# Kernel tuning notes

Hardware: AMD Instinct MI355X
Metric: run time of the kernel (lower is better)

Reference implementation:

```python
import jax, jax.numpy as jnp
import numpy as np

B, T, M, S, D, H, DH, P = 4, 1024, 1024, 1024, 1024, 16, 64, 4096


def layernorm(x, g, b, eps=1e-5):
    mu = x.mean(-1, keepdims=True)
    var = ((x - mu) ** 2).mean(-1, keepdims=True)
    return (x - mu) * jax.lax.rsqrt(var + eps) * g + b


def rel_shift(x):
    # Transformer-XL relative shift on [B,H,q,k] BD scores
    b, h, q, k = x.shape
    x = jnp.pad(x, ((0, 0), (0, 0), (0, 0), (1, 0)))
    return x.reshape(b, h, k + 1, q)[:, :, 1:, :].reshape(b, h, q, k)


def rel_attention(x, kv, mem, mask, pos_emb, r_w_bias, r_r_bias,
                  Wq, Wk, Wv, Wr, Wo, g, bln):
    # x: [B,Tq,D] queries; kv: [B,Skv,D]; mem: optional [B,M,D]
    cat = kv if mem is None else jnp.concatenate([mem, kv], axis=1)
    Bb, Tq, _ = x.shape
    K = cat.shape[1]
    q = (x @ Wq).reshape(Bb, Tq, H, DH)
    k = (cat @ Wk).reshape(Bb, K, H, DH)
    v = (cat @ Wv).reshape(Bb, K, H, DH)
    r = (pos_emb[-K:] @ Wr).reshape(K, H, DH)  # rel-pos keys, most-recent K positions
    AC = jnp.einsum('bthd,bkhd->bhtk', q + r_w_bias, k)
    BD = rel_shift(jnp.einsum('bthd,khd->bhtk', q + r_r_bias, r))
    scores = (AC + BD) * (1.0 / np.sqrt(DH))
    scores = jnp.where(mask[:, None, :, :], jnp.asarray(-1e30, scores.dtype), scores)
    prob = jax.nn.softmax(scores, axis=-1)
    o = jnp.einsum('bhtk,bkhd->bthd', prob, v).reshape(Bb, Tq, H * DH) @ Wo
    return layernorm(x + o, g, bln), cat, prob  # post-LN residual; cat is new memory


def residual_ff(x, W1, b1, W2, b2, g, bln):
    h = jax.nn.relu(x @ W1 + b1) @ W2 + b2
    return layernorm(x + h, g, bln)


def setup_inputs() -> dict:
    key = jax.random.key(0)
    ks = jax.random.split(key, 24)
    w = lambda i, shape: jax.random.normal(ks[i], shape, jnp.float32) * 0.02
    causal = jnp.triu(jnp.ones((T, M + T), bool), k=M + 1)  # True = masked
    return {
        'src': jax.random.normal(ks[0], (B, S, D), jnp.float32),
        'tgt': jax.random.normal(ks[1], (B, T, D), jnp.float32),
        'tgt_mem': jax.random.normal(ks[2], (B, M, D), jnp.float32),
        'pos_emb': w(3, (M + T, D)),
        'r_w_bias': w(4, (H, DH)),
        'r_r_bias': w(5, (H, DH)),
        'Wq1': w(6, (D, H * DH)), 'Wk1': w(7, (D, H * DH)), 'Wv1': w(8, (D, H * DH)),
        'Wr1': w(9, (D, H * DH)), 'Wo1': w(10, (H * DH, D)),
        'ln1_g': jnp.ones((D,), jnp.float32), 'ln1_b': jnp.zeros((D,), jnp.float32),
        'Wq2': w(11, (D, H * DH)), 'Wk2': w(12, (D, H * DH)), 'Wv2': w(13, (D, H * DH)),
        'Wr2': w(14, (D, H * DH)), 'Wo2': w(15, (H * DH, D)),
        'ln2_g': jnp.ones((D,), jnp.float32), 'ln2_b': jnp.zeros((D,), jnp.float32),
        'Wf1': w(16, (D, P)), 'bf1': jnp.zeros((P,), jnp.float32),
        'Wf2': w(17, (P, D)), 'bf2': jnp.zeros((D,), jnp.float32),
        'ln3_g': jnp.ones((D,), jnp.float32), 'ln3_b': jnp.zeros((D,), jnp.float32),
        'tgt_mask': jnp.broadcast_to(causal, (B, T, M + T)),
        'tgt_to_src_mask': jnp.zeros((B, T, S), bool),
    }


def reference(src, tgt, tgt_mem, pos_emb, r_w_bias, r_r_bias,
              Wq1, Wk1, Wv1, Wr1, Wo1, ln1_g, ln1_b,
              Wq2, Wk2, Wv2, Wr2, Wo2, ln2_g, ln2_b,
              Wf1, bf1, Wf2, bf2, ln3_g, ln3_b,
              tgt_mask, tgt_to_src_mask):
    out, new_mem, self_att_prob = rel_attention(
        tgt, tgt, tgt_mem, tgt_mask, pos_emb, r_w_bias, r_r_bias,
        Wq1, Wk1, Wv1, Wr1, Wo1, ln1_g, ln1_b)
    out, _, inter_att_prob = rel_attention(
        out, src, None, tgt_to_src_mask, pos_emb, r_w_bias, r_r_bias,
        Wq2, Wk2, Wv2, Wr2, Wo2, ln2_g, ln2_b)
    out = residual_ff(out, Wf1, bf1, Wf2, bf2, ln3_g, ln3_b)
    return (out, new_mem, self_att_prob, inter_att_prob)
```

## Files before the change

kernel.cpp:

```cpp
#include <hip/hip_runtime.h>

typedef unsigned short u16;
typedef __attribute__((ext_vector_type(8))) short short8;
typedef __attribute__((ext_vector_type(4))) float f4;
typedef __attribute__((ext_vector_type(4))) unsigned short u16x4;

__device__ __forceinline__ float b2f(u16 u) {
    unsigned int x = ((unsigned int)u) << 16;
    return __builtin_bit_cast(float, x);
}
__device__ __forceinline__ u16 f2b(float f) {
    unsigned int u = __builtin_bit_cast(unsigned int, f);
    u += 0x7FFFu + ((u >> 16) & 1u);
    return (u16)(u >> 16);
}

__device__ __forceinline__ void gl16(const void* g, void* l) {
    __builtin_amdgcn_global_load_lds(
        (const __attribute__((address_space(1))) void*)g,
        (__attribute__((address_space(3))) void*)l, 16, 0, 0);
}

template<int FM, int FN, int CBF, int EPI>
__global__ __launch_bounds__(256, 3)
void gemm_bt(const u16* __restrict__ Ap, const u16* __restrict__ Bp,
             void* __restrict__ Cp, const float* __restrict__ bias,
             int M, int N, int K, int lda, int ldb, int ldc,
             long long sAh, long long sAb, long long sBh, long long sBb,
             long long sCh, long long sCb, int batchH)
{
    constexpr int BM = FM * 32;
    constexpr int BN = FN * 32;
    __shared__ __align__(16) u16 As[BM * 32];
    __shared__ __align__(16) u16 Bs[BN * 32];

    const int tid  = threadIdx.x;
    const int z    = blockIdx.z;
    const int bb   = z / batchH;
    const int hh   = z - bb * batchH;
    const int m0   = blockIdx.y * BM;
    const int n0   = blockIdx.x * BN;
    const int w    = tid >> 6;
    const int lane = tid & 63;
    const int wr   = w >> 1;
    const int wc   = w & 1;
    const int lrow = lane & 15;
    const int lk   = (lane >> 4) << 3;
    const int lrow4 = lane >> 2;
    const int lch   = lane & 3;

    const u16* Ag = Ap + sAb * bb + sAh * hh;
    const u16* Bg = Bp + sBb * bb + sBh * hh;

    f4 acc[FM][FN] = {};

    const int nKt = K >> 5;
    for (int kt = 0; kt < nKt; ++kt) {
        const int kb = kt << 5;
        __syncthreads();
        #pragma unroll
        for (int i = 0; i < BM / 64; ++i) {
            const int row0 = (w + i * 4) << 4;
            gl16(Ag + (long long)(m0 + row0 + lrow4) * lda + kb + (lch << 3),
                 &As[row0 * 32]);
        }
        #pragma unroll
        for (int i = 0; i < BN / 64; ++i) {
            const int row0 = (w + i * 4) << 4;
            gl16(Bg + (long long)(n0 + row0 + lrow4) * ldb + kb + (lch << 3),
                 &Bs[row0 * 32]);
        }
        __syncthreads();

        short8 af[FM], bv[FN];
        #pragma unroll
        for (int m = 0; m < FM; ++m)
            af[m] = *(const short8*)(&As[(wr * FM * 16 + m * 16 + lrow) * 32 + lk]);
        #pragma unroll
        for (int n = 0; n < FN; ++n)
            bv[n] = *(const short8*)(&Bs[(wc * FN * 16 + n * 16 + lrow) * 32 + lk]);
        #pragma unroll
        for (int m = 0; m < FM; ++m)
            #pragma unroll
            for (int n = 0; n < FN; ++n)
                acc[m][n] = __builtin_amdgcn_mfma_f32_16x16x32_bf16(af[m], bv[n], acc[m][n], 0, 0, 0);
    }

    const int crow0 = m0 + wr * FM * 16 + ((lane >> 4) << 2);
    const int ccol0 = n0 + wc * FN * 16 + lrow;
    if (CBF == 0) {
        float* Cg = (float*)Cp + sCb * bb + sCh * hh;
        #pragma unroll
        for (int m = 0; m < FM; ++m) {
            #pragma unroll
            for (int n = 0; n < FN; ++n) {
                const int col = ccol0 + n * 16;
                float bvv = (EPI >= 1) ? bias[col] : 0.f;
                #pragma unroll
                for (int r = 0; r < 4; ++r) {
                    float vv = acc[m][n][r] + bvv;
                    if (EPI == 2) vv = fmaxf(vv, 0.f);
                    Cg[(long long)(crow0 + m * 16 + r) * ldc + col] = vv;
                }
            }
        }
    } else {
        u16* Cg = (u16*)Cp + sCb * bb + sCh * hh;
        #pragma unroll
        for (int m = 0; m < FM; ++m) {
            #pragma unroll
            for (int n = 0; n < FN; ++n) {
                const int col = ccol0 + n * 16;
                float bvv = (EPI >= 1) ? bias[col] : 0.f;
                #pragma unroll
                for (int r = 0; r < 4; ++r) {
                    float vv = acc[m][n][r] + bvv;
                    if (EPI == 2) vv = fmaxf(vv, 0.f);
                    Cg[(long long)(crow0 + m * 16 + r) * ldc + col] = f2b(vv);
                }
            }
        }
    }
}

template<int KK, int MODE>
__global__ __launch_bounds__(512)
void fattn(const u16* __restrict__ qw, const u16* __restrict__ qr,
           const u16* __restrict__ kb, const u16* __restrict__ rr,
           const u16* __restrict__ vt,
           float* __restrict__ probs, u16* __restrict__ ob, int kld)
{
    constexpr int LE = KK + 8;
    constexpr int NT = KK / 16;
    __shared__ __align__(16) u16 e[16 * LE];
    __shared__ __align__(16) u16 qws[16 * 72];
    __shared__ __align__(16) u16 qrs[17 * 72];
    __shared__ float psum[8][16];

    const int tid = threadIdx.x;
    const int bh  = blockIdx.y;
    const int b   = bh >> 4, h = bh & 15;
    const int t0  = blockIdx.x << 4;

    if (tid < 128) {
        const int row = tid >> 3, ch = tid & 7;
        *(short8*)&qws[row * 72 + ch * 8] =
            *(const short8*)(qw + ((long long)(b * 1024 + t0 + row)) * 1024 + h * 64 + ch * 8);
    } else if (tid < 256) {
        const int row = (tid - 128) >> 3, ch = tid & 7;
        *(short8*)&qrs[row * 72 + ch * 8] =
            *(const short8*)(qr + ((long long)(b * 1024 + t0 + row)) * 1024 + h * 64 + ch * 8);
    } else if (MODE == 1 && tid < 264) {
        const int ch = tid - 256;
        const int trow = (t0 + 16 > 1023) ? 1023 : (t0 + 16);
        *(short8*)&qrs[16 * 72 + ch * 8] =
            *(const short8*)(qr + ((long long)(b * 1024 + trow)) * 1024 + h * 64 + ch * 8);
    }
    __syncthreads();

    const int w = tid >> 6, lane = tid & 63;
    const int lc = lane & 15, g = lane >> 4, lk = g << 3;
    const int t = t0 + lc;

    const short8 bq0 = *(const short8*)&qws[lc * 72 + lk];
    const short8 bq1 = *(const short8*)&qws[lc * 72 + 32 + lk];
    const short8 br0 = *(const short8*)&qrs[lc * 72 + lk];
    const short8 br1 = *(const short8*)&qrs[lc * 72 + 32 + lk];
    short8 bs0 = {}, bs1 = {};
    if (MODE == 1) {
        bs0 = *(const short8*)&qrs[(lc + 1) * 72 + lk];
        bs1 = *(const short8*)&qrs[(lc + 1) * 72 + 32 + lk];
    }

    for (int ut = w; ut < NT; ut += 8) {
        const int u0 = ut << 4;
        const bool need1 = (u0 + t0 + 30 >= 1023);
        const bool need2 = (MODE == 1) && (u0 + t0 <= 1021);
        if (!need1 && !need2) continue;
        const u16* rg = rr + (long long)(u0 + lc) * 2048 + h * 64;
        const short8 a0 = *(const short8*)(rg + lk);
        const short8 a1 = *(const short8*)(rg + 32 + lk);
        if (need1) {
            f4 acc = {};
            acc = __builtin_amdgcn_mfma_f32_16x16x32_bf16(a0, br0, acc, 0, 0, 0);
            acc = __builtin_amdgcn_mfma_f32_16x16x32_bf16(a1, br1, acc, 0, 0, 0);
            #pragma unroll
            for (int i = 0; i < 4; ++i) {
                const int j = u0 + 4 * g + i + t - 1023;
                if (j >= 0) e[lc * LE + j] = f2b(acc[i]);
            }
        }
        if (MODE == 1 && need2) {
            f4 acc = {};
            acc = __builtin_amdgcn_mfma_f32_16x16x32_bf16(a0, bs0, acc, 0, 0, 0);
            acc = __builtin_amdgcn_mfma_f32_16x16x32_bf16(a1, bs1, acc, 0, 0, 0);
            #pragma unroll
            for (int i = 0; i < 4; ++i) {
                const int j = u0 + 4 * g + i + t + 2;
                if (j < KK) e[lc * LE + j] = f2b(acc[i]);
            }
        }
    }
    __syncthreads();

    float sum = 0.f;
    const int limit = t + 1024;
    const int jvt = (MODE == 0) ? ((t0 + 1039) >> 4) : (NT - 1);
    #pragma unroll 2
    for (int jt = w; jt < NT; jt += 8) {
        const int j0 = jt << 4;
        const int jme = j0 + 4 * g;
        if (MODE == 0 && jt > jvt) {
            u16x4 z = {0, 0, 0, 0};
            *(u16x4*)&e[lc * LE + jme] = z;
            continue;
        }
        const u16* kg = kb + (long long)(b * KK + j0 + lc) * kld + h * 64;
        const short8 a0 = *(const short8*)(kg + lk);
        const short8 a1 = *(const short8*)(kg + 32 + lk);
        f4 acc = {};
        acc = __builtin_amdgcn_mfma_f32_16x16x32_bf16(a0, bq0, acc, 0, 0, 0);
        acc = __builtin_amdgcn_mfma_f32_16x16x32_bf16(a1, bq1, acc, 0, 0, 0);
        u16x4 bd4 = *(const u16x4*)&e[lc * LE + jme];
        u16x4 st;
        #pragma unroll
        for (int i = 0; i < 4; ++i) {
            const int j = jme + i;
            float bd = b2f(bd4[i]);
            if (MODE == 1 && j == t + 1) bd = 0.f;
            float ev = __expf(acc[i] + bd);
            if (MODE == 0 && j > limit) ev = 0.f;
            sum += ev;
            st[i] = f2b(ev);
        }
        *(u16x4*)&e[lc * LE + jme] = st;
    }
    sum += __shfl_xor(sum, 16);
    sum += __shfl_xor(sum, 32);
    if (g == 0) psum[w][lc] = sum;
    __syncthreads();

    if (w >= 4) {
        const int r = (tid >> 4) & 15;
        const int q = tid & 15;
        float s = 0.f;
        #pragma unroll
        for (int w2 = 0; w2 < 8; ++w2) s += psum[w2][r];
        const float inv = 1.f / s;
        float* pr = probs + ((long long)bh * 1024 + t0 + r) * KK;
        #pragma unroll 4
        for (int i2 = 0; i2 < KK / 128; ++i2) {
            const int j0 = q * 8 + i2 * 128;
            u16x4 e0 = *(const u16x4*)&e[r * LE + j0];
            u16x4 e1 = *(const u16x4*)&e[r * LE + j0 + 4];
            f4 p0, p1;
            p0.x = b2f(e0.x) * inv; p0.y = b2f(e0.y) * inv;
            p0.z = b2f(e0.z) * inv; p0.w = b2f(e0.w) * inv;
            p1.x = b2f(e1.x) * inv; p1.y = b2f(e1.y) * inv;
            p1.z = b2f(e1.z) * inv; p1.w = b2f(e1.w) * inv;
            *(f4*)(pr + j0) = p0;
            *(f4*)(pr + j0 + 4) = p1;
        }
    } else {
        const int db = w << 4;
        const u16* vrow = vt + ((long long)(bh * 64 + db + lc)) * KK + lk;
        int kcend = KK / 32;
        if (MODE == 0) {
            const int ke = (t0 + 1071) >> 5;
            if (ke < kcend) kcend = ke;
        }
        f4 acc = {};
        #pragma unroll 2
        for (int kc = 0; kc < kcend; ++kc) {
            short8 a = *(const short8*)&e[lc * LE + kc * 32 + lk];
            short8 bv = *(const short8*)(vrow + kc * 32);
            acc = __builtin_amdgcn_mfma_f32_16x16x32_bf16(a, bv, acc, 0, 0, 0);
        }
        #pragma unroll
        for (int i = 0; i < 4; ++i) {
            const int trow = g * 4 + i;
            float s = 0.f;
            #pragma unroll
            for (int w2 = 0; w2 < 8; ++w2) s += psum[w2][trow];
            ob[((long long)(b * 1024 + t0 + trow)) * 1024 + h * 64 + db + lc] = f2b(acc[i] / s);
        }
    }
}

__global__ void conv_f2b(const float* __restrict__ in, u16* __restrict__ out, long long n4)
{
    long long i = (long long)blockIdx.x * 256 + threadIdx.x;
    if (i >= n4) return;
    f4 v = *(const f4*)(in + i * 4);
    u16x4 o; o.x = f2b(v.x); o.y = f2b(v.y); o.z = f2b(v.z); o.w = f2b(v.w);
    *(u16x4*)(out + i * 4) = o;
}

__global__ void concat_mem(const float* __restrict__ mem, const float* __restrict__ tgt,
                           float* __restrict__ nm, u16* __restrict__ cat)
{
    long long i = (long long)blockIdx.x * 256 + threadIdx.x;
    long long b = i >> 19;
    int rem = (int)(i & 524287);
    int r = rem >> 8, c4 = rem & 255;
    const float* sp = (r < 1024) ? (mem + ((b << 10) + r) * 1024 + c4 * 4)
                                 : (tgt + ((b << 10) + (r - 1024)) * 1024 + c4 * 4);
    f4 v = *(const f4*)sp;
    *(f4*)(nm + i * 4) = v;
    u16x4 o; o.x = f2b(v.x); o.y = f2b(v.y); o.z = f2b(v.z); o.w = f2b(v.w);
    *(u16x4*)(cat + i * 4) = o;
}

struct TW10 { const float* s[10]; u16* d[10]; };
__global__ void transpose_w10(TW10 p)
{
    __shared__ float tile[32][33];
    const float* W = p.s[blockIdx.z];
    u16* Wt = p.d[blockIdx.z];
    int c0 = blockIdx.x * 32, r0 = blockIdx.y * 32;
    int tx = threadIdx.x, ty = threadIdx.y;
    tile[ty][tx] = W[(long long)(r0 + ty) * 1024 + c0 + tx];
    __syncthreads();
    Wt[(long long)(c0 + ty) * 1024 + r0 + tx] = f2b(tile[tx][ty]);
}

__global__ void transpose_w(const float* __restrict__ W, u16* __restrict__ Wt, int R, int C)
{
    __shared__ float tile[32][33];
    int c0 = blockIdx.x * 32, r0 = blockIdx.y * 32;
    int tx = threadIdx.x, ty = threadIdx.y;
    tile[ty][tx] = W[(long long)(r0 + ty) * C + c0 + tx];
    __syncthreads();
    Wt[(long long)(c0 + ty) * R + r0 + tx] = f2b(tile[tx][ty]);
}

__global__ void transpose_v(const u16* __restrict__ v, u16* __restrict__ vt,
                            int KK, int ld, int coff)
{
    __shared__ u16 tile[32][33];
    int z = blockIdx.z; int b = z >> 4, hh = z & 15;
    int j0 = blockIdx.x * 32, d0 = blockIdx.y * 32;
    int tx = threadIdx.x, ty = threadIdx.y;
    tile[ty][tx] = v[((long long)(b * KK + j0 + ty)) * ld + coff + hh * 64 + d0 + tx];
    __syncthreads();
    vt[((long long)((b * 16 + hh) * 64 + d0 + ty)) * KK + j0 + tx] = tile[tx][ty];
}

__global__ void add_qbias(const u16* __restrict__ src, long long ld, long long sb,
                          const float* __restrict__ rwb, const float* __restrict__ rrb,
                          u16* __restrict__ qwo, u16* __restrict__ qro)
{
    long long i = (long long)blockIdx.x * 256 + threadIdx.x;
    const int col = (int)((i * 4) & 1023);
    const long long trow = (i * 4) >> 10;
    const long long b = trow >> 10;
    const long long tr = trow & 1023;
    u16x4 qq = *(const u16x4*)(src + b * sb + tr * ld + col);
    f4 wv = *(const f4*)(rwb + col);
    f4 rv = *(const f4*)(rrb + col);
    u16x4 a, c;
    a.x = f2b((b2f(qq.x) + wv.x) * 0.125f); a.y = f2b((b2f(qq.y) + wv.y) * 0.125f);
    a.z = f2b((b2f(qq.z) + wv.z) * 0.125f); a.w = f2b((b2f(qq.w) + wv.w) * 0.125f);
    c.x = f2b((b2f(qq.x) + rv.x) * 0.125f); c.y = f2b((b2f(qq.y) + rv.y) * 0.125f);
    c.z = f2b((b2f(qq.z) + rv.z) * 0.125f); c.w = f2b((b2f(qq.w) + rv.w) * 0.125f);
    *(u16x4*)(qwo + i * 4) = a;
    *(u16x4*)(qro + i * 4) = c;
}

__global__ __launch_bounds__(256) void ln_res(const float* __restrict__ x,
                                              const float* __restrict__ h1,
                                              const float* __restrict__ h2,
                                              const float* __restrict__ hbias,
                                              const float* __restrict__ g, const float* __restrict__ bl,
                                              float* __restrict__ o32, u16* __restrict__ obf)
{
    const long long row = blockIdx.x;
    const int tid = threadIdx.x;
    const long long base = row * 1024 + tid * 4;
    f4 xa = *(const f4*)(x + base);
    f4 ha = *(const f4*)(h1 + base);
    f4 hb = *(const f4*)(h2 + base);
    f4 hc = {0.f, 0.f, 0.f, 0.f};
    if (hbias) hc = *(const f4*)(hbias + tid * 4);
    float v0 = xa.x + ha.x + hb.x + hc.x, v1 = xa.y + ha.y + hb.y + hc.y;
    float v2 = xa.z + ha.z + hb.z + hc.z, v3 = xa.w + ha.w + hb.w + hc.w;
    float lsum = v0 + v1 + v2 + v3;
    float lsq = v0 * v0 + v1 * v1 + v2 * v2 + v3 * v3;
    #pragma unroll
    for (int o2 = 32; o2; o2 >>= 1) { lsum += __shfl_xor(lsum, o2); lsq += __shfl_xor(lsq, o2); }
    __shared__ float r1[4], r2[4];
    int w = tid >> 6, lane = tid & 63;
    if (lane == 0) { r1[w] = lsum; r2[w] = lsq; }
    __syncthreads();
    lsum = r1[0] + r1[1] + r1[2] + r1[3];
    lsq  = r2[0] + r2[1] + r2[2] + r2[3];
    const float mu = lsum * 0.0009765625f;
    const float var = lsq * 0.0009765625f - mu * mu;
    const float rsd = rsqrtf(var + 1e-5f);
    const int c = tid * 4;
    f4 gv = *(const f4*)(g + c);
    f4 bv = *(const f4*)(bl + c);
    f4 y;
    y.x = (v0 - mu) * rsd * gv.x + bv.x;
    y.y = (v1 - mu) * rsd * gv.y + bv.y;
    y.z = (v2 - mu) * rsd * gv.z + bv.z;
    y.w = (v3 - mu) * rsd * gv.w + bv.w;
    *(f4*)(o32 + base) = y;
    if (obf) {
        u16x4 u; u.x = f2b(y.x); u.y = f2b(y.y); u.z = f2b(y.z); u.w = f2b(y.w);
        *(u16x4*)(obf + base) = u;
    }
}

extern "C" void kernel_launch(void* const* d_in, const int* in_sizes, int n_in,
                              void* d_out, int out_size, void* d_ws, size_t ws_size,
                              hipStream_t stream)
{
    (void)in_sizes; (void)n_in; (void)out_size;
    const float* src  = (const float*)d_in[0];
    const float* tgt  = (const float*)d_in[1];
    const float* mem  = (const float*)d_in[2];
    const float* pos  = (const float*)d_in[3];
    const float* rwb  = (const float*)d_in[4];
    const float* rrb  = (const float*)d_in[5];
    const float* Wq1  = (const float*)d_in[6];
    const float* Wk1  = (const float*)d_in[7];
    const float* Wv1  = (const float*)d_in[8];
    const float* Wr1  = (const float*)d_in[9];
    const float* Wo1  = (const float*)d_in[10];
    const float* ln1g = (const float*)d_in[11];
    const float* ln1b = (const float*)d_in[12];
    const float* Wq2  = (const float*)d_in[13];
    const float* Wk2  = (const float*)d_in[14];
    const float* Wv2  = (const float*)d_in[15];
    const float* Wr2  = (const float*)d_in[16];
    const float* Wo2  = (const float*)d_in[17];
    const float* ln2g = (const float*)d_in[18];
    const float* ln2b = (const float*)d_in[19];
    const float* Wf1  = (const float*)d_in[20];
    const float* bf1  = (const float*)d_in[21];
    const float* Wf2  = (const float*)d_in[22];
    const float* bf2  = (const float*)d_in[23];
    const float* ln3g = (const float*)d_in[24];
    const float* ln3b = (const float*)d_in[25];

    float* outp   = (float*)d_out;
    float* newmem = outp + 4194304;
    float* selfP  = outp + 12582912;
    float* interP = outp + 146800640;

    char* ws = (char*)d_ws;
    size_t off = 0;
    auto alloc = [&](size_t bytes) -> void* {
        void* p = ws + off;
        off = (off + bytes + 255) & ~(size_t)255;
        return p;
    };
    u16*   src_bf  = (u16*)alloc(8u << 20);
    u16*   cat_bf  = (u16*)alloc(16u << 20);
    u16*   pos_bf  = (u16*)alloc(4u << 20);
    u16*   W1t    = (u16*)alloc(6u << 20);
    u16*   Wr12t  = (u16*)alloc(4u << 20);
    u16*   W2t    = (u16*)alloc(4u << 20);
    u16*   Wq2t   = (u16*)alloc(2u << 20);
    u16*   Wo1t   = (u16*)alloc(2u << 20);
    u16*   Wo2t   = (u16*)alloc(2u << 20);
    u16*   Wf1t   = (u16*)alloc(8u << 20);
    u16*   Wf2t   = (u16*)alloc(8u << 20);
    u16*   P1     = (u16*)alloc(48u << 20);
    u16*   P2     = (u16*)alloc(16u << 20);
    u16*   R12    = (u16*)alloc(8u << 20);
    u16*   qwb    = (u16*)alloc(8u << 20);
    u16*   qrb    = (u16*)alloc(8u << 20);
    u16*   qb2    = (u16*)alloc(8u << 20);
    u16*   vtb    = (u16*)alloc(16u << 20);
    u16*   ob     = (u16*)alloc(8u << 20);
    float* projb  = (float*)alloc(16u << 20);
    float* projb2 = (float*)alloc(16u << 20);
    float* out1_32 = (float*)alloc(16u << 20);
    u16*   out1_bf = (u16*)alloc(8u << 20);
    float* out2_32 = (float*)alloc(16u << 20);
    u16*   out2_bf = (u16*)alloc(8u << 20);
    u16*   hb     = (u16*)alloc(32u << 20);
    if (off > ws_size) return;
    const long long PJ2 = projb2 - projb;

    dim3 tb(32, 32);

    concat_mem<<<8192, 256, 0, stream>>>(mem, tgt, newmem, cat_bf);
    conv_f2b<<<4096, 256, 0, stream>>>(src, src_bf, 1048576);
    conv_f2b<<<2048, 256, 0, stream>>>(pos, pos_bf, 524288);
    TW10 tw;
    tw.s[0] = Wq1; tw.d[0] = W1t;
    tw.s[1] = Wk1; tw.d[1] = W1t + 1048576;
    tw.s[2] = Wv1; tw.d[2] = W1t + 2097152;
    tw.s[3] = Wr1; tw.d[3] = Wr12t;
    tw.s[4] = Wr2; tw.d[4] = Wr12t + 1048576;
    tw.s[5] = Wk2; tw.d[5] = W2t;
    tw.s[6] = Wv2; tw.d[6] = W2t + 1048576;
    tw.s[7] = Wq2; tw.d[7] = Wq2t;
    tw.s[8] = Wo1; tw.d[8] = Wo1t;
    tw.s[9] = Wo2; tw.d[9] = Wo2t;
    transpose_w10<<<dim3(32, 32, 10), tb, 0, stream>>>(tw);
    transpose_w<<<dim3(128, 32), tb, 0, stream>>>(Wf1, Wf1t, 1024, 4096);
    transpose_w<<<dim3(32, 128), tb, 0, stream>>>(Wf2, Wf2t, 4096, 1024);

    gemm_bt<4,4,1,0><<<dim3(24,64,1), 256, 0, stream>>>(cat_bf, W1t, P1, nullptr,
        8192,3072,1024, 1024,1024,3072, 0,0,0,0,0,0, 1);
    gemm_bt<4,4,1,0><<<dim3(16,16,1), 256, 0, stream>>>(pos_bf, Wr12t, R12, nullptr,
        2048,2048,1024, 1024,1024,2048, 0,0,0,0,0,0, 1);
    add_qbias<<<4096, 256, 0, stream>>>(P1 + 1024LL * 3072, 3072LL, 2048LL * 3072,
                                        rwb, rrb, qwb, qrb);
    transpose_v<<<dim3(64,2,64), tb, 0, stream>>>(P1, vtb, 2048, 3072, 2048);
    fattn<2048,0><<<dim3(64,64), 512, 0, stream>>>(qwb, qrb, P1 + 1024, R12, vtb,
                                                   selfP, ob, 3072);
    gemm_bt<4,4,0,0><<<dim3(8,32,2), 256, 0, stream>>>(ob, Wo1t, projb, nullptr,
        4096,1024,512, 1024,1024,1024, 0,512, 0,512, 0,PJ2, 1);
    ln_res<<<4096, 256, 0, stream>>>(tgt, projb, projb2, nullptr, ln1g, ln1b, out1_32, out1_bf);

    gemm_bt<4,4,1,0><<<dim3(8,32,1), 256, 0, stream>>>(out1_bf, Wq2t, qb2, nullptr,
        4096,1024,1024, 1024,1024,1024, 0,0,0,0,0,0, 1);
    gemm_bt<4,4,1,0><<<dim3(16,32,1), 256, 0, stream>>>(src_bf, W2t, P2, nullptr,
        4096,2048,1024, 1024,1024,2048, 0,0,0,0,0,0, 1);
    add_qbias<<<4096, 256, 0, stream>>>(qb2, 1024LL, 1048576LL, rwb, rrb, qwb, qrb);
    transpose_v<<<dim3(32,2,64), tb, 0, stream>>>(P2, vtb, 1024, 2048, 1024);
    fattn<1024,1><<<dim3(64,64), 512, 0, stream>>>(qwb, qrb, P2,
        R12 + 1024LL * 2048 + 1024, vtb, interP, ob, 2048);
    gemm_bt<4,4,0,0><<<dim3(8,32,2), 256, 0, stream>>>(ob, Wo2t, projb, nullptr,
        4096,1024,512, 1024,1024,1024, 0,512, 0,512, 0,PJ2, 1);
    ln_res<<<4096, 256, 0, stream>>>(out1_32, projb, projb2, nullptr, ln2g, ln2b, out2_32, out2_bf);

    gemm_bt<4,4,1,2><<<dim3(32,32,1), 256, 0, stream>>>(out2_bf, Wf1t, hb, bf1,
        4096,4096,1024, 1024,1024,4096, 0,0,0,0,0,0, 1);
    gemm_bt<4,4,0,0><<<dim3(8,32,2), 256, 0, stream>>>(hb, Wf2t, projb, nullptr,
        4096,1024,2048, 4096,4096,1024, 0,2048, 0,2048, 0,PJ2, 1);
    ln_res<<<4096, 256, 0, stream>>>(out2_32, projb, projb2, bf2, ln3g, ln3b, outp, nullptr);
}
```

Baseline: 1.043 ms.

## Fuse q-bias into attention, batch weight transposes, widen V transpose tiles

The add_qbias pass is folded into the attention kernel's query staging, so the q+bias tensors are no longer written to and re-read from global memory. The separate weight-transpose launches become one 18-slice launch, and the second layer's Q, K and V projections run as one batched GEMM launch. The V transpose now uses 64x64 tiles with 16-byte vector accesses. Prob and new-memory stores become nontemporal, and unroll factors in the attention loops are raised. In exchange there is more register pressure and more work in the attention prologue.

```diff
diff --git a/kernel.cpp b/kernel.cpp
--- a/kernel.cpp
+++ b/kernel.cpp
@@ -125,7 +125,8 @@
 
 template<int KK, int MODE>
 __global__ __launch_bounds__(512)
-void fattn(const u16* __restrict__ qw, const u16* __restrict__ qr,
+void fattn(const u16* __restrict__ qsrc, long long qld, long long qsb,
+           const float* __restrict__ rwb, const float* __restrict__ rrb,
            const u16* __restrict__ kb, const u16* __restrict__ rr,
            const u16* __restrict__ vt,
            float* __restrict__ probs, u16* __restrict__ ob, int kld)
@@ -142,19 +143,28 @@
     const int b   = bh >> 4, h = bh & 15;
     const int t0  = blockIdx.x << 4;
 
-    if (tid < 128) {
-        const int row = tid >> 3, ch = tid & 7;
-        *(short8*)&qws[row * 72 + ch * 8] =
-            *(const short8*)(qw + ((long long)(b * 1024 + t0 + row)) * 1024 + h * 64 + ch * 8);
-    } else if (tid < 256) {
-        const int row = (tid - 128) >> 3, ch = tid & 7;
-        *(short8*)&qrs[row * 72 + ch * 8] =
-            *(const short8*)(qr + ((long long)(b * 1024 + t0 + row)) * 1024 + h * 64 + ch * 8);
-    } else if (MODE == 1 && tid < 264) {
-        const int ch = tid - 256;
-        const int trow = (t0 + 16 > 1023) ? 1023 : (t0 + 16);
-        *(short8*)&qrs[16 * 72 + ch * 8] =
-            *(const short8*)(qr + ((long long)(b * 1024 + trow)) * 1024 + h * 64 + ch * 8);
+    if (tid < 264) {
+        int row, ch; const float* bias; u16* dst; bool act = true;
+        if (tid < 128)      { row = tid >> 3;        ch = tid & 7; bias = rwb; dst = &qws[row * 72 + ch * 8]; }
+        else if (tid < 256) { row = (tid - 128) >> 3; ch = tid & 7; bias = rrb; dst = &qrs[row * 72 + ch * 8]; }
+        else if (MODE == 1) { row = 16;              ch = tid - 256; bias = rrb; dst = &qrs[16 * 72 + ch * 8]; }
+        else act = false;
+        if (act) {
+            int trow = t0 + row; if (trow > 1023) trow = 1023;
+            short8 qv = *(const short8*)(qsrc + b * qsb + (long long)trow * qld + h * 64 + ch * 8);
+            const float* bp = bias + h * 64 + ch * 8;
+            f4 b0 = *(const f4*)bp, b1 = *(const f4*)(bp + 4);
+            short8 o;
+            o[0] = (short)f2b((b2f((u16)qv[0]) + b0.x) * 0.125f);
+            o[1] = (short)f2b((b2f((u16)qv[1]) + b0.y) * 0.125f);
+            o[2] = (short)f2b((b2f((u16)qv[2]) + b0.z) * 0.125f);
+            o[3] = (short)f2b((b2f((u16)qv[3]) + b0.w) * 0.125f);
+            o[4] = (short)f2b((b2f((u16)qv[4]) + b1.x) * 0.125f);
+            o[5] = (short)f2b((b2f((u16)qv[5]) + b1.y) * 0.125f);
+            o[6] = (short)f2b((b2f((u16)qv[6]) + b1.z) * 0.125f);
+            o[7] = (short)f2b((b2f((u16)qv[7]) + b1.w) * 0.125f);
+            *(short8*)dst = o;
+        }
     }
     __syncthreads();
 
@@ -172,6 +182,7 @@
         bs1 = *(const short8*)&qrs[(lc + 1) * 72 + 32 + lk];
     }
 
+    #pragma unroll 2
     for (int ut = w; ut < NT; ut += 8) {
         const int u0 = ut << 4;
         const bool need1 = (u0 + t0 + 30 >= 1023);
@@ -206,7 +217,7 @@
     float sum = 0.f;
     const int limit = t + 1024;
     const int jvt = (MODE == 0) ? ((t0 + 1039) >> 4) : (NT - 1);
-    #pragma unroll 2
+    #pragma unroll 4
     for (int jt = w; jt < NT; jt += 8) {
         const int j0 = jt << 4;
         const int jme = j0 + 4 * g;
@@ -258,8 +269,8 @@
             p0.z = b2f(e0.z) * inv; p0.w = b2f(e0.w) * inv;
             p1.x = b2f(e1.x) * inv; p1.y = b2f(e1.y) * inv;
             p1.z = b2f(e1.z) * inv; p1.w = b2f(e1.w) * inv;
-            *(f4*)(pr + j0) = p0;
-            *(f4*)(pr + j0 + 4) = p1;
+            __builtin_nontemporal_store(p0, (f4*)(pr + j0));
+            __builtin_nontemporal_store(p1, (f4*)(pr + j0 + 4));
         }
     } else {
         const int db = w << 4;
@@ -306,65 +317,48 @@
     const float* sp = (r < 1024) ? (mem + ((b << 10) + r) * 1024 + c4 * 4)
                                  : (tgt + ((b << 10) + (r - 1024)) * 1024 + c4 * 4);
     f4 v = *(const f4*)sp;
-    *(f4*)(nm + i * 4) = v;
+    __builtin_nontemporal_store(v, (f4*)(nm + i * 4));
     u16x4 o; o.x = f2b(v.x); o.y = f2b(v.y); o.z = f2b(v.z); o.w = f2b(v.w);
     *(u16x4*)(cat + i * 4) = o;
 }
 
-struct TW10 { const float* s[10]; u16* d[10]; };
-__global__ void transpose_w10(TW10 p)
+struct TWS { const float* s; u16* d; int sld, dld; };
+struct TW18 { TWS t[18]; };
+__global__ void transpose_w18(TW18 p)
 {
     __shared__ float tile[32][33];
-    const float* W = p.s[blockIdx.z];
-    u16* Wt = p.d[blockIdx.z];
+    const TWS ts = p.t[blockIdx.z];
     int c0 = blockIdx.x * 32, r0 = blockIdx.y * 32;
     int tx = threadIdx.x, ty = threadIdx.y;
-    tile[ty][tx] = W[(long long)(r0 + ty) * 1024 + c0 + tx];
+    tile[ty][tx] = ts.s[(long long)(r0 + ty) * ts.sld + c0 + tx];
     __syncthreads();
-    Wt[(long long)(c0 + ty) * 1024 + r0 + tx] = f2b(tile[tx][ty]);
-}
-
-__global__ void transpose_w(const float* __restrict__ W, u16* __restrict__ Wt, int R, int C)
-{
-    __shared__ float tile[32][33];
-    int c0 = blockIdx.x * 32, r0 = blockIdx.y * 32;
-    int tx = threadIdx.x, ty = threadIdx.y;
-    tile[ty][tx] = W[(long long)(r0 + ty) * C + c0 + tx];
+    ts.d[(long long)(c0 + ty) * ts.dld + r0 + tx] = f2b(tile[tx][ty]);
+}
+
+__global__ __launch_bounds__(256) void transpose_v(const u16* __restrict__ v, u16* __restrict__ vt,
+                                                   int KK, int ld, int coff)
+{
+    __shared__ u16 tile[64][68];
+    const int z = blockIdx.z, b = z >> 4, h = z & 15;
+    const int j0 = blockIdx.x << 6;
+    const int rr8 = threadIdx.x >> 3;
+    const int c8 = (threadIdx.x & 7) << 3;
+    #pragma unroll
+    for (int p = 0; p < 2; ++p) {
+        const int jr = p * 32 + rr8;
+        short8 val = *(const short8*)(v + ((long long)(b * KK + j0 + jr)) * ld + coff + h * 64 + c8);
+        #pragma unroll
+        for (int k = 0; k < 8; ++k) tile[c8 + k][jr] = (u16)val[k];
+    }
     __syncthreads();
-    Wt[(long long)(c0 + ty) * R + r0 + tx] = f2b(tile[tx][ty]);
-}
-
-__global__ void transpose_v(const u16* __restrict__ v, u16* __restrict__ vt,
-                            int KK, int ld, int coff)
-{
-    __shared__ u16 tile[32][33];
-    int z = blockIdx.z; int b = z >> 4, hh = z & 15;
-    int j0 = blockIdx.x * 32, d0 = blockIdx.y * 32;
-    int tx = threadIdx.x, ty = threadIdx.y;
-    tile[ty][tx] = v[((long long)(b * KK + j0 + ty)) * ld + coff + hh * 64 + d0 + tx];
-    __syncthreads();
-    vt[((long long)((b * 16 + hh) * 64 + d0 + ty)) * KK + j0 + tx] = tile[tx][ty];
-}
-
-__global__ void add_qbias(const u16* __restrict__ src, long long ld, long long sb,
-                          const float* __restrict__ rwb, const float* __restrict__ rrb,
-                          u16* __restrict__ qwo, u16* __restrict__ qro)
-{
-    long long i = (long long)blockIdx.x * 256 + threadIdx.x;
-    const int col = (int)((i * 4) & 1023);
-    const long long trow = (i * 4) >> 10;
-    const long long b = trow >> 10;
-    const long long tr = trow & 1023;
-    u16x4 qq = *(const u16x4*)(src + b * sb + tr * ld + col);
-    f4 wv = *(const f4*)(rwb + col);
-    f4 rv = *(const f4*)(rrb + col);
-    u16x4 a, c;
-    a.x = f2b((b2f(qq.x) + wv.x) * 0.125f); a.y = f2b((b2f(qq.y) + wv.y) * 0.125f);
-    a.z = f2b((b2f(qq.z) + wv.z) * 0.125f); a.w = f2b((b2f(qq.w) + wv.w) * 0.125f);
-    c.x = f2b((b2f(qq.x) + rv.x) * 0.125f); c.y = f2b((b2f(qq.y) + rv.y) * 0.125f);
-    c.z = f2b((b2f(qq.z) + rv.z) * 0.125f); c.w = f2b((b2f(qq.w) + rv.w) * 0.125f);
-    *(u16x4*)(qwo + i * 4) = a;
-    *(u16x4*)(qro + i * 4) = c;
+    #pragma unroll
+    for (int p = 0; p < 2; ++p) {
+        const int d = p * 32 + rr8;
+        short8 o;
+        #pragma unroll
+        for (int k = 0; k < 8; ++k) o[k] = (short)tile[d][c8 + k];
+        *(short8*)(vt + ((long long)((b * 16 + h) * 64 + d)) * KK + j0 + c8) = o;
+    }
 }
 
 __global__ __launch_bounds__(256) void ln_res(const float* __restrict__ x,
@@ -468,10 +462,9 @@
     u16*   Wf1t   = (u16*)alloc(8u << 20);
     u16*   Wf2t   = (u16*)alloc(8u << 20);
     u16*   P1     = (u16*)alloc(48u << 20);
-    u16*   P2     = (u16*)alloc(16u << 20);
+    u16*   P2k    = (u16*)alloc(8u << 20);
+    u16*   P2v    = (u16*)alloc(8u << 20);
     u16*   R12    = (u16*)alloc(8u << 20);
-    u16*   qwb    = (u16*)alloc(8u << 20);
-    u16*   qrb    = (u16*)alloc(8u << 20);
     u16*   qb2    = (u16*)alloc(8u << 20);
     u16*   vtb    = (u16*)alloc(16u << 20);
     u16*   ob     = (u16*)alloc(8u << 20);
@@ -490,42 +483,46 @@
     concat_mem<<<8192, 256, 0, stream>>>(mem, tgt, newmem, cat_bf);
     conv_f2b<<<4096, 256, 0, stream>>>(src, src_bf, 1048576);
     conv_f2b<<<2048, 256, 0, stream>>>(pos, pos_bf, 524288);
-    TW10 tw;
-    tw.s[0] = Wq1; tw.d[0] = W1t;
-    tw.s[1] = Wk1; tw.d[1] = W1t + 1048576;
-    tw.s[2] = Wv1; tw.d[2] = W1t + 2097152;
-    tw.s[3] = Wr1; tw.d[3] = Wr12t;
-    tw.s[4] = Wr2; tw.d[4] = Wr12t + 1048576;
-    tw.s[5] = Wk2; tw.d[5] = W2t;
-    tw.s[6] = Wv2; tw.d[6] = W2t + 1048576;
-    tw.s[7] = Wq2; tw.d[7] = Wq2t;
-    tw.s[8] = Wo1; tw.d[8] = Wo1t;
-    tw.s[9] = Wo2; tw.d[9] = Wo2t;
-    transpose_w10<<<dim3(32, 32, 10), tb, 0, stream>>>(tw);
-    transpose_w<<<dim3(128, 32), tb, 0, stream>>>(Wf1, Wf1t, 1024, 4096);
-    transpose_w<<<dim3(32, 128), tb, 0, stream>>>(Wf2, Wf2t, 4096, 1024);
+    TW18 tw;
+    tw.t[0] = {Wq1, W1t, 1024, 1024};
+    tw.t[1] = {Wk1, W1t + 1048576, 1024, 1024};
+    tw.t[2] = {Wv1, W1t + 2097152, 1024, 1024};
+    tw.t[3] = {Wr1, Wr12t, 1024, 1024};
+    tw.t[4] = {Wr2, Wr12t + 1048576, 1024, 1024};
+    tw.t[5] = {Wk2, W2t, 1024, 1024};
+    tw.t[6] = {Wv2, W2t + 1048576, 1024, 1024};
+    tw.t[7] = {Wq2, Wq2t, 1024, 1024};
+    tw.t[8] = {Wo1, Wo1t, 1024, 1024};
+    tw.t[9] = {Wo2, Wo2t, 1024, 1024};
+    for (int zz = 0; zz < 4; ++zz) {
+        tw.t[10 + zz] = {Wf1 + zz * 1024, Wf1t + (long long)zz * 1048576, 4096, 1024};
+        tw.t[14 + zz] = {Wf2 + (long long)zz * 1048576, Wf2t + zz * 1024, 1024, 4096};
+    }
+    transpose_w18<<<dim3(32, 32, 18), tb, 0, stream>>>(tw);
 
     gemm_bt<4,4,1,0><<<dim3(24,64,1), 256, 0, stream>>>(cat_bf, W1t, P1, nullptr,
         8192,3072,1024, 1024,1024,3072, 0,0,0,0,0,0, 1);
     gemm_bt<4,4,1,0><<<dim3(16,16,1), 256, 0, stream>>>(pos_bf, Wr12t, R12, nullptr,
         2048,2048,1024, 1024,1024,2048, 0,0,0,0,0,0, 1);
-    add_qbias<<<4096, 256, 0, stream>>>(P1 + 1024LL * 3072, 3072LL, 2048LL * 3072,
-                                        rwb, rrb, qwb, qrb);
-    transpose_v<<<dim3(64,2,64), tb, 0, stream>>>(P1, vtb, 2048, 3072, 2048);
-    fattn<2048,0><<<dim3(64,64), 512, 0, stream>>>(qwb, qrb, P1 + 1024, R12, vtb,
-                                                   selfP, ob, 3072);
+    transpose_v<<<dim3(32,1,64), 256, 0, stream>>>(P1, vtb, 2048, 3072, 2048);
+    fattn<2048,0><<<dim3(64,64), 512, 0, stream>>>(P1 + 1024LL * 3072, 3072LL, 2048LL * 3072,
+        rwb, rrb, P1 + 1024, R12, vtb, selfP, ob, 3072);
     gemm_bt<4,4,0,0><<<dim3(8,32,2), 256, 0, stream>>>(ob, Wo1t, projb, nullptr,
         4096,1024,512, 1024,1024,1024, 0,512, 0,512, 0,PJ2, 1);
     ln_res<<<4096, 256, 0, stream>>>(tgt, projb, projb2, nullptr, ln1g, ln1b, out1_32, out1_bf);
 
-    gemm_bt<4,4,1,0><<<dim3(8,32,1), 256, 0, stream>>>(out1_bf, Wq2t, qb2, nullptr,
-        4096,1024,1024, 1024,1024,1024, 0,0,0,0,0,0, 1);
-    gemm_bt<4,4,1,0><<<dim3(16,32,1), 256, 0, stream>>>(src_bf, W2t, P2, nullptr,
-        4096,2048,1024, 1024,1024,2048, 0,0,0,0,0,0, 1);
-    add_qbias<<<4096, 256, 0, stream>>>(qb2, 1024LL, 1048576LL, rwb, rrb, qwb, qrb);
-    transpose_v<<<dim3(32,2,64), tb, 0, stream>>>(P2, vtb, 1024, 2048, 1024);
-    fattn<1024,1><<<dim3(64,64), 512, 0, stream>>>(qwb, qrb, P2,
-        R12 + 1024LL * 2048 + 1024, vtb, interP, ob, 2048);
+    {
+        const long long dA = (long long)(src_bf - out1_bf);
+        const long long dB1 = (long long)(W2t - Wq2t);
+        const long long dB2 = (long long)((W2t + 1048576) - Wq2t);
+        const long long dC1 = (long long)(P2k - qb2);
+        const long long dC2 = (long long)(P2v - qb2);
+        gemm_bt<4,4,1,0><<<dim3(8,32,3), 256, 0, stream>>>(out1_bf, Wq2t, qb2, nullptr,
+            4096,1024,1024, 1024,1024,1024, dA,dA, dB1,dB2, dC1,dC2, 2);
+    }
+    transpose_v<<<dim3(16,1,64), 256, 0, stream>>>(P2v, vtb, 1024, 1024, 0);
+    fattn<1024,1><<<dim3(64,64), 512, 0, stream>>>(qb2, 1024LL, 1048576LL,
+        rwb, rrb, P2k, R12 + 1024LL * 2048 + 1024, vtb, interP, ob, 1024);
     gemm_bt<4,4,0,0><<<dim3(8,32,2), 256, 0, stream>>>(ob, Wo2t, projb, nullptr,
         4096,1024,512, 1024,1024,1024, 0,512, 0,512, 0,PJ2, 1);
     ln_res<<<4096, 256, 0, stream>>>(out1_32, projb, projb2, nullptr, ln2g, ln2b, out2_32, out2_bf);
```

After: 971.7 us. -6.8%, faster.
